# Optimization experiments

Measured on AMD Instinct MI355X. Metric: run time of the kernel, lower is better.

The kernel has to match this reference:

```python
import jax, jax.numpy as jnp
import numpy as np

B, CIN, COUT, T, J = 64, 128, 128, 128, 25
EPS = 1e-5  # BatchNorm2d default eps


def setup_inputs() -> dict:
    key = jax.random.key(0)
    k = jax.random.split(key, 5)
    x = jax.random.normal(k[0], (B, CIN, T, J), jnp.float32)
    adj = jax.random.normal(k[1], (J, J), jnp.float32) / np.sqrt(J).astype(np.float32)
    Wk = jax.random.normal(k[2], (COUT, CIN), jnp.float32) / np.sqrt(CIN).astype(np.float32)
    Wq = jax.random.normal(k[3], (COUT, CIN), jnp.float32) / np.sqrt(CIN).astype(np.float32)
    Ws = jax.random.normal(k[4], (COUT, CIN), jnp.float32) / np.sqrt(CIN).astype(np.float32)
    return {
        "x": x, "adj": adj,
        "Wk": Wk, "bk": jnp.zeros((COUT,), jnp.float32),
        "Wq": Wq, "bq": jnp.zeros((COUT,), jnp.float32),
        "Ws": Ws, "bs": jnp.zeros((COUT,), jnp.float32),
        "gamma": jnp.ones((COUT,), jnp.float32),
        "beta": jnp.zeros((COUT,), jnp.float32),
        "run_mean": jnp.zeros((COUT,), jnp.float32),
        "run_var": jnp.ones((COUT,), jnp.float32),
        "alpha": jnp.ones((1,), jnp.float32),
    }


def reference(x, adj, Wk, bk, Wq, bq, Ws, bs, gamma, beta, run_mean, run_var, alpha):
    # static graph conv: aggregate over joints with the shared adjacency
    static = jnp.einsum('bctj,jk->bctk', x, adj)              # [B,Cin,T,J]
    # 1x1 conv == channel matmul
    static_feat = jnp.einsum('oc,bctj->botj', Ws, static) + bs[None, :, None, None]  # [B,Cout,T,J]
    # temporal mean pooling, then key/query 1x1 convs
    x_t = x.mean(axis=2)                                      # [B,Cin,J]
    kk = jnp.einsum('oc,bcj->boj', Wk, x_t) + bk[None, :, None]  # [B,Cout,J]
    qq = jnp.einsum('oc,bcj->boj', Wq, x_t) + bq[None, :, None]  # [B,Cout,J]
    # attention-style dynamic adjacency: softmax(q^T k / sqrt(Cout)) over last axis
    scale = jnp.sqrt(jnp.asarray(kk.shape[1], x.dtype))
    scores = jnp.einsum('bcj,bck->bjk', qq, kk) / scale       # [B,J,J]
    dyn = jax.nn.softmax(scores, axis=-1)                     # [B,J,J]
    # original expands dyn to (B*T, Cout, J, J); same math without materialization:
    dyn_feat = jnp.einsum('bctj,bjk->bctk', static_feat, dyn)  # [B,Cout,T,J]
    out = static_feat + alpha[0] * dyn_feat
    # BatchNorm2d in inference mode (running stats), then ReLU
    inv = gamma[None, :, None, None] * jax.lax.rsqrt(run_var[None, :, None, None] + EPS)
    out = (out - run_mean[None, :, None, None]) * inv + beta[None, :, None, None]
    return jax.nn.relu(out)
```

## Files before the change

kernel.cpp:

```cpp
#include <hip/hip_runtime.h>

#define B_ 64
#define C_ 128
#define T_ 128
#define J_ 25
#define PIT 136
#define XP 40
#define GP 136
#define TT 4

typedef unsigned short ushort_t;
typedef __attribute__((ext_vector_type(8))) unsigned short ushort8;
typedef __attribute__((ext_vector_type(4))) unsigned short ushort4_t;
typedef __attribute__((ext_vector_type(8))) _Float16 half8;
typedef __attribute__((ext_vector_type(4))) float f32x4;
typedef float f32x4u __attribute__((ext_vector_type(4), aligned(4)));
typedef unsigned short ushort8u __attribute__((ext_vector_type(8), aligned(2)));

__device__ __forceinline__ float bf2f(ushort_t u) {
  unsigned int v = ((unsigned int)u) << 16;
  return __builtin_bit_cast(float, v);
}
__device__ __forceinline__ ushort_t f2bf(float f) {
  unsigned int u = __builtin_bit_cast(unsigned int, f);
  u += 0x7FFFu + ((u >> 16) & 1u);
  return (ushort_t)(u >> 16);
}
__device__ __forceinline__ ushort_t f2h_bits(float f) {
  _Float16 h = (_Float16)f;
  return __builtin_bit_cast(ushort_t, h);
}
__device__ __forceinline__ float h2f(ushort_t u) {
  return (float)__builtin_bit_cast(_Float16, u);
}
__device__ __forceinline__ half8 cvt_bf8_h8(ushort8 u) {
  half8 r;
#pragma unroll
  for (int i = 0; i < 8; ++i) r[i] = (_Float16)bf2f(u[i]);
  return r;
}
__device__ __forceinline__ float ldv(const void* p, long i, int isf32) {
  return isf32 ? ((const float*)p)[i] : bf2f(((const ushort_t*)p)[i]);
}
__device__ __forceinline__ half8 ld8h(const void* p, long i, int isf32) {
  half8 r;
  if (isf32) {
    const float* f = (const float*)p + i;
#pragma unroll
    for (int k = 0; k < 8; ++k) r[k] = (_Float16)f[k];
  } else {
    ushort8 u = *(const ushort8*)((const ushort_t*)p + i);
    r = cvt_bf8_h8(u);
  }
  return r;
}

__device__ __forceinline__ int detect_isf32(const void* p, int tid) {
  const ushort_t* u = (const ushort_t*)p;
  float a = fabsf(bf2f(u[2 * (tid & 63)]));
  int ok = (a > 1e-4f && a < 64.f) ? 1 : 0;
  unsigned long long m = __ballot(ok);
  return (__popcll(m) > 32) ? 0 : 1;
}

__global__ __launch_bounds__(256) void k_mean(const void* __restrict__ x,
                                              float* __restrict__ xt) {
  const int bc = blockIdx.x;
  const int b = bc >> 7, c = bc & 127;
  const long base = (long)bc * 3200;
  const int tid = threadIdx.x;
  const int isf32 = detect_isf32((const ushort_t*)x + base, tid);
  __shared__ float pl[3200];
  __shared__ float red[8][32];
  if (isf32) {
    const f32x4* src = (const f32x4*)((const float*)x + base);
    for (int i = tid; i < 800; i += 256) *(f32x4*)&pl[i * 4] = src[i];
  } else {
    const ushort4_t* src = (const ushort4_t*)((const ushort_t*)x + base);
    for (int i = tid; i < 800; i += 256) {
      ushort4_t u = src[i];
      f32x4 v;
#pragma unroll
      for (int r = 0; r < 4; ++r) v[r] = bf2f(u[r]);
      *(f32x4*)&pl[i * 4] = v;
    }
  }
  __syncthreads();
  const int j = tid & 31, g = tid >> 5;
  float s = 0.f;
  if (j < J_) {
#pragma unroll
    for (int i = 0; i < 16; ++i) s += pl[(g * 16 + i) * 25 + j];
  }
  red[g][j] = s;
  __syncthreads();
  if (tid < 32) {
    float tot = 0.f;
#pragma unroll
    for (int gg = 0; gg < 8; ++gg) tot += red[gg][tid];
    if (tid < J_) xt[b * 4096 + tid * 128 + c] = tot * (1.0f / 128.0f);
  }
}

__global__ __launch_bounds__(256) void k_attn(
    const float* __restrict__ xt, const void* __restrict__ adj,
    const void* __restrict__ Wk, const void* __restrict__ bk,
    const void* __restrict__ Wq, const void* __restrict__ bq,
    const void* __restrict__ alphap, ushort_t* __restrict__ fkws,
    float* __restrict__ sws) {
  const int b = blockIdx.x;
  const int tid = threadIdx.x;
  const int isf32 = detect_isf32(Wk, tid);
  const int wv = tid >> 6, lane = tid & 63, lrow = lane & 15, quad = lane >> 4;
  const float alpha = ldv(alphap, 0, isf32);

  __shared__ __align__(16) ushort_t xtT[32 * PIT];
  __shared__ __align__(16) ushort_t kkT[32 * PIT];
  __shared__ __align__(16) ushort_t qqT[32 * PIT];
  __shared__ float sc[32 * 33];

  for (int idx = tid; idx < 32 * PIT; idx += 256) {
    int r = idx / PIT, col = idx % PIT;
    float v = (r < J_ && col < 128) ? xt[b * 4096 + r * 128 + col] : 0.f;
    xtT[idx] = f2h_bits(v);
  }
  __syncthreads();

  for (int mat = 0; mat < 2; ++mat) {
    const void* W = mat ? Wq : Wk;
    const void* bias = mat ? bq : bk;
    ushort_t* dstT = mat ? qqT : kkT;
    f32x4 acc[2][2] = {};
    for (int ks = 0; ks < 4; ++ks) {
      half8 bfr[2];
#pragma unroll
      for (int jt = 0; jt < 2; ++jt)
        bfr[jt] = *(const half8*)&xtT[(jt * 16 + lrow) * PIT + ks * 32 + quad * 8];
#pragma unroll
      for (int ot = 0; ot < 2; ++ot) {
        int o = (2 * wv + ot) * 16 + lrow;
        half8 afr = ld8h(W, o * 128 + ks * 32 + quad * 8, isf32);
#pragma unroll
        for (int jt = 0; jt < 2; ++jt)
          acc[ot][jt] = __builtin_amdgcn_mfma_f32_16x16x32_f16(afr, bfr[jt],
                                                               acc[ot][jt], 0, 0, 0);
      }
    }
#pragma unroll
    for (int ot = 0; ot < 2; ++ot) {
      int obase = (2 * wv + ot) * 16 + quad * 4;
#pragma unroll
      for (int jt = 0; jt < 2; ++jt) {
        int j = jt * 16 + lrow;
        ushort_t pack[4];
#pragma unroll
        for (int r = 0; r < 4; ++r)
          pack[r] = f2h_bits(acc[ot][jt][r] + ldv(bias, obase + r, isf32));
        *(ushort4_t*)&dstT[j * PIT + obase] = *(ushort4_t*)pack;
      }
    }
  }
  __syncthreads();

  {
    const int mt = wv >> 1, nt = wv & 1;
    f32x4 acc = {};
    for (int ks = 0; ks < 4; ++ks) {
      half8 afr = *(const half8*)&qqT[(mt * 16 + lrow) * PIT + ks * 32 + quad * 8];
      half8 bfr = *(const half8*)&kkT[(nt * 16 + lrow) * PIT + ks * 32 + quad * 8];
      acc = __builtin_amdgcn_mfma_f32_16x16x32_f16(afr, bfr, acc, 0, 0, 0);
    }
    const float rs = 0.08838834764831845f;
#pragma unroll
    for (int r = 0; r < 4; ++r)
      sc[(mt * 16 + quad * 4 + r) * 33 + nt * 16 + lrow] = acc[r] * rs;
  }
  __syncthreads();

  if (tid < J_) {
    float m = -1e30f;
    for (int k = 0; k < J_; ++k) m = fmaxf(m, sc[tid * 33 + k]);
    float sum = 0.f;
    for (int k = 0; k < J_; ++k) {
      float e = expf(sc[tid * 33 + k] - m);
      sc[tid * 33 + k] = e;
      sum += e;
    }
    float inv = 1.f / sum;
    for (int k = 0; k < J_; ++k) sc[tid * 33 + k] *= inv;
  }
  __syncthreads();

  for (int idx = tid; idx < 1280; idx += 256) {
    int k = idx / XP, jj = idx % XP;
    float v = 0.f;
    if (k < J_ && jj < J_) {
      v = ldv(adj, jj * J_ + k, isf32);
      float d = 0.f;
      for (int m = 0; m < J_; ++m) d += ldv(adj, jj * J_ + m, isf32) * sc[m * 33 + k];
      v += alpha * d;
    }
    fkws[b * 1280 + idx] = f2h_bits(v);
  }
  if (tid < 32) {
    float v = 0.f;
    if (tid < J_) {
      float d = 0.f;
      for (int jj = 0; jj < J_; ++jj) d += sc[jj * 33 + tid];
      v = 1.f + alpha * d;
    }
    sws[b * 32 + tid] = v;
  }
}

#define SM_FK 0
#define SM_GT 2560
#define SM_TOT 33024
__global__ __launch_bounds__(256, 4) void k_main(
    const void* __restrict__ x, const void* __restrict__ Ws,
    const void* __restrict__ bs, const void* __restrict__ gamma,
    const void* __restrict__ beta, const void* __restrict__ rmean,
    const void* __restrict__ rvar, const ushort_t* __restrict__ fkws,
    const float* __restrict__ sws, void* __restrict__ out) {
  const int tid = threadIdx.x;
  const int isf32 = detect_isf32(Ws, tid);
  const int b = blockIdx.x >> 5, tb = blockIdx.x & 31, t0 = tb * TT;
  const int wv = tid >> 6, lane = tid & 63, lrow = lane & 15, quad = lane >> 4;

  __shared__ __align__(16) char smem[SM_TOT];
  __shared__ float bnscale[128], bnshift[128], bsv[128], sv[32];
  ushort_t* fk = (ushort_t*)(smem + SM_FK);
  ushort_t* gt = (ushort_t*)(smem + SM_GT);
  ushort_t* outbuf = (ushort_t*)(smem + SM_GT);

  half8 wsf[2][4];
#pragma unroll
  for (int ot = 0; ot < 2; ++ot) {
    int o = (2 * wv + ot) * 16 + lrow;
#pragma unroll
    for (int ks = 0; ks < 4; ++ks)
      wsf[ot][ks] = ld8h(Ws, o * 128 + ks * 32 + quad * 8, isf32);
  }

  for (int i = tid; i < 160; i += 256)
    *(ushort8*)&fk[i * 8] = *(const ushort8*)&fkws[b * 1280 + i * 8];
  for (int i = tid; i < 204; i += 256) {
    int row = 100 + i / 17, col8 = (i % 17) * 8;
    ushort8 z = {};
    *(ushort8*)&gt[row * GP + col8] = z;
  }
  if (tid < 32) sv[tid] = sws[b * 32 + tid];
  if (tid < 128) {
    float g = ldv(gamma, tid, isf32), v = ldv(rvar, tid, isf32);
    float scl = g * rsqrtf(v + 1e-5f);
    bnscale[tid] = scl;
    bnshift[tid] = ldv(beta, tid, isf32) - ldv(rmean, tid, isf32) * scl;
    bsv[tid] = ldv(bs, tid, isf32);
  }
  __syncthreads();

  {
    half8 afr[2];
#pragma unroll
    for (int mt = 0; mt < 2; ++mt)
      afr[mt] = *(const half8*)&fk[(mt * 16 + lrow) * XP + quad * 8];
    const float* xf = (const float*)x;
    const ushort_t* xh = (const ushort_t*)x;
#pragma unroll
    for (int t = 0; t < TT; ++t) {
#pragma unroll
      for (int ci = 0; ci < 2; ++ci) {
        int ct = 2 * wv + ci;
        long p = (long)b * 409600 + (long)(ct * 16 + lrow) * 3200 + (t0 + t) * 25;
        half8 bfr;
        if (quad < 3) {
          if (isf32) {
            f32x4u v0 = *(const f32x4u*)(xf + p + quad * 8);
            f32x4u v1 = *(const f32x4u*)(xf + p + quad * 8 + 4);
#pragma unroll
            for (int r = 0; r < 4; ++r) {
              bfr[r] = (_Float16)v0[r];
              bfr[4 + r] = (_Float16)v1[r];
            }
          } else {
            ushort8u u = *(const ushort8u*)(xh + p + quad * 8);
#pragma unroll
            for (int r = 0; r < 8; ++r) bfr[r] = (_Float16)bf2f(u[r]);
          }
        } else {
          bfr = (half8){};
          bfr[0] = (_Float16)(isf32 ? xf[p + 24] : bf2f(xh[p + 24]));
        }
        f32x4 accg[2] = {};
#pragma unroll
        for (int mt = 0; mt < 2; ++mt)
          accg[mt] = __builtin_amdgcn_mfma_f32_16x16x32_f16(afr[mt], bfr, accg[mt], 0, 0, 0);
#pragma unroll
        for (int mt = 0; mt < 2; ++mt)
#pragma unroll
          for (int r = 0; r < 4; ++r) {
            int kk = mt * 16 + quad * 4 + r;
            if (kk < J_)
              gt[(t * 25 + kk) * GP + ct * 16 + lrow] = f2h_bits(accg[mt][r]);
          }
      }
    }
  }
  __syncthreads();

  f32x4 acc[2][7];
#pragma unroll
  for (int ot = 0; ot < 2; ++ot)
#pragma unroll
    for (int nt = 0; nt < 7; ++nt) acc[ot][nt] = (f32x4){};
  for (int ks = 0; ks < 4; ++ks) {
#pragma unroll
    for (int nt = 0; nt < 7; ++nt) {
      half8 bfr = *(const half8*)&gt[(nt * 16 + lrow) * GP + ks * 32 + quad * 8];
#pragma unroll
      for (int ot = 0; ot < 2; ++ot)
        acc[ot][nt] = __builtin_amdgcn_mfma_f32_16x16x32_f16(wsf[ot][ks], bfr,
                                                             acc[ot][nt], 0, 0, 0);
    }
  }
  __syncthreads();

#pragma unroll
  for (int nt = 0; nt < 7; ++nt) {
    int n = nt * 16 + lrow;
    if (n < 100) {
      float svk = sv[n % 25];
#pragma unroll
      for (int ot = 0; ot < 2; ++ot) {
        int obase = (2 * wv + ot) * 16 + quad * 4;
#pragma unroll
        for (int r = 0; r < 4; ++r) {
          int o = obase + r;
          float v = acc[ot][nt][r] + bsv[o] * svk;
          v = v * bnscale[o] + bnshift[o];
          outbuf[o * 100 + n] = f2h_bits(fmaxf(v, 0.f));
        }
      }
    }
  }
  __syncthreads();

  {
    const long obase = ((long)(b * 128) * 128 + t0) * 25;
    if (isf32) {
      float* of = (float*)out + obase;
      for (int idx = tid; idx < 3200; idx += 256) {
        int o = idx / 25, q = idx % 25;
        ushort4_t u = *(const ushort4_t*)&outbuf[o * 100 + q * 4];
        f32x4 v;
#pragma unroll
        for (int r = 0; r < 4; ++r) v[r] = h2f(u[r]);
        *(f32x4*)(of + (long)o * 3200 + q * 4) = v;
      }
    } else {
      ushort_t* oh = (ushort_t*)out + obase;
      for (int idx = tid; idx < 3200; idx += 256) {
        int o = idx / 25, q = idx % 25;
        ushort4_t u = *(const ushort4_t*)&outbuf[o * 100 + q * 4];
        ushort4_t w;
#pragma unroll
        for (int r = 0; r < 4; ++r) w[r] = f2bf(h2f(u[r]));
        *(ushort4_t*)(oh + (long)o * 3200 + q * 4) = w;
      }
    }
  }
}

extern "C" void kernel_launch(void* const* d_in, const int* in_sizes, int n_in,
                              void* d_out, int out_size, void* d_ws, size_t ws_size,
                              hipStream_t stream) {
  const void* x = d_in[0];
  const void* adj = d_in[1];
  const void* Wk = d_in[2];
  const void* bk = d_in[3];
  const void* Wq = d_in[4];
  const void* bq = d_in[5];
  const void* Ws = d_in[6];
  const void* bsp = d_in[7];
  const void* gamma = d_in[8];
  const void* beta = d_in[9];
  const void* rmean = d_in[10];
  const void* rvar = d_in[11];
  const void* alphap = d_in[12];

  char* ws = (char*)d_ws;
  float* xt = (float*)ws;
  ushort_t* fkws = (ushort_t*)(ws + 64 * 4096 * 4);
  float* sws = (float*)(ws + 64 * 4096 * 4 + 64 * 1280 * 2);

  k_mean<<<B_ * C_, 256, 0, stream>>>(x, xt);
  k_attn<<<B_, 256, 0, stream>>>(xt, adj, Wk, bk, Wq, bq, alphap, fkws, sws);
  k_main<<<B_ * (T_ / TT), 256, 0, stream>>>(x, Ws, bsp, gamma, beta, rmean, rvar,
                                             fkws, sws, d_out);
}
```

Baseline: 300.0 us.

## Halve k_main time tile, prefetch x, write output directly from MFMA accumulators

k_main now handles 2 timesteps per block instead of 4, which doubles the grid and shrinks shared memory so the launch bound can request 6 blocks per CU. The x fragments are loaded into registers before the fk/BN setup so global latency overlaps the setup work. The second MFMA swaps its operands so each lane owns one output channel, letting the epilogue apply bias, BN and ReLU and store straight to global memory, removing the outbuf staging and two barriers. The xt workspace is stored as fp16, so k_attn can read it with vector loads. Trade-offs: more blocks reload the Ws fragments and fkws, and the direct stores are narrower and less coalesced than the old staged writes.

Result: slower. 316.7 us (+5.6%).

```diff
diff --git a/kernel.cpp b/kernel.cpp
--- a/kernel.cpp
+++ b/kernel.cpp
@@ -7,7 +7,7 @@
 #define PIT 136
 #define XP 40
 #define GP 136
-#define TT 4
+#define TT 2
 
 typedef unsigned short ushort_t;
 typedef __attribute__((ext_vector_type(8))) unsigned short ushort8;
@@ -16,6 +16,7 @@
 typedef __attribute__((ext_vector_type(4))) float f32x4;
 typedef float f32x4u __attribute__((ext_vector_type(4), aligned(4)));
 typedef unsigned short ushort8u __attribute__((ext_vector_type(8), aligned(2)));
+typedef unsigned short ushort4u __attribute__((ext_vector_type(4), aligned(2)));
 
 __device__ __forceinline__ float bf2f(ushort_t u) {
   unsigned int v = ((unsigned int)u) << 16;
@@ -64,7 +65,7 @@
 }
 
 __global__ __launch_bounds__(256) void k_mean(const void* __restrict__ x,
-                                              float* __restrict__ xt) {
+                                              ushort_t* __restrict__ xt) {
   const int bc = blockIdx.x;
   const int b = bc >> 7, c = bc & 127;
   const long base = (long)bc * 3200;
@@ -98,12 +99,12 @@
     float tot = 0.f;
 #pragma unroll
     for (int gg = 0; gg < 8; ++gg) tot += red[gg][tid];
-    if (tid < J_) xt[b * 4096 + tid * 128 + c] = tot * (1.0f / 128.0f);
+    if (tid < J_) xt[b * 4096 + tid * 128 + c] = f2h_bits(tot * (1.0f / 128.0f));
   }
 }
 
 __global__ __launch_bounds__(256) void k_attn(
-    const float* __restrict__ xt, const void* __restrict__ adj,
+    const ushort_t* __restrict__ xt, const void* __restrict__ adj,
     const void* __restrict__ Wk, const void* __restrict__ bk,
     const void* __restrict__ Wq, const void* __restrict__ bq,
     const void* __restrict__ alphap, ushort_t* __restrict__ fkws,
@@ -119,10 +120,11 @@
   __shared__ __align__(16) ushort_t qqT[32 * PIT];
   __shared__ float sc[32 * 33];
 
-  for (int idx = tid; idx < 32 * PIT; idx += 256) {
-    int r = idx / PIT, col = idx % PIT;
-    float v = (r < J_ && col < 128) ? xt[b * 4096 + r * 128 + col] : 0.f;
-    xtT[idx] = f2h_bits(v);
+  for (int idx = tid; idx < 32 * 17; idx += 256) {
+    int r = idx / 17, c8 = idx % 17;
+    ushort8 v = {};
+    if (r < J_ && c8 < 16) v = *(const ushort8*)&xt[b * 4096 + r * 128 + c8 * 8];
+    *(ushort8*)&xtT[r * PIT + c8 * 8] = v;
   }
   __syncthreads();
 
@@ -215,8 +217,8 @@
 
 #define SM_FK 0
 #define SM_GT 2560
-#define SM_TOT 33024
-__global__ __launch_bounds__(256, 4) void k_main(
+#define SM_TOT (2560 + 64 * GP * 2)
+__global__ __launch_bounds__(256, 6) void k_main(
     const void* __restrict__ x, const void* __restrict__ Ws,
     const void* __restrict__ bs, const void* __restrict__ gamma,
     const void* __restrict__ beta, const void* __restrict__ rmean,
@@ -224,14 +226,13 @@
     const float* __restrict__ sws, void* __restrict__ out) {
   const int tid = threadIdx.x;
   const int isf32 = detect_isf32(Ws, tid);
-  const int b = blockIdx.x >> 5, tb = blockIdx.x & 31, t0 = tb * TT;
+  const int b = blockIdx.x >> 6, tb = blockIdx.x & 63, t0 = tb * TT;
   const int wv = tid >> 6, lane = tid & 63, lrow = lane & 15, quad = lane >> 4;
 
   __shared__ __align__(16) char smem[SM_TOT];
   __shared__ float bnscale[128], bnshift[128], bsv[128], sv[32];
   ushort_t* fk = (ushort_t*)(smem + SM_FK);
   ushort_t* gt = (ushort_t*)(smem + SM_GT);
-  ushort_t* outbuf = (ushort_t*)(smem + SM_GT);
 
   half8 wsf[2][4];
 #pragma unroll
@@ -242,12 +243,44 @@
       wsf[ot][ks] = ld8h(Ws, o * 128 + ks * 32 + quad * 8, isf32);
   }
 
+  half8 xa[TT][2];
+  {
+    const float* xf = (const float*)x;
+    const ushort_t* xh = (const ushort_t*)x;
+#pragma unroll
+    for (int t = 0; t < TT; ++t)
+#pragma unroll
+      for (int ci = 0; ci < 2; ++ci) {
+        const int ct = 2 * wv + ci;
+        const long p = (long)b * 409600 + (long)(ct * 16 + lrow) * 3200 + (t0 + t) * 25;
+        half8 bfr;
+        if (quad < 3) {
+          if (isf32) {
+            f32x4u v0 = *(const f32x4u*)(xf + p + quad * 8);
+            f32x4u v1 = *(const f32x4u*)(xf + p + quad * 8 + 4);
+#pragma unroll
+            for (int r = 0; r < 4; ++r) {
+              bfr[r] = (_Float16)v0[r];
+              bfr[4 + r] = (_Float16)v1[r];
+            }
+          } else {
+            ushort8u u = *(const ushort8u*)(xh + p + quad * 8);
+#pragma unroll
+            for (int r = 0; r < 8; ++r) bfr[r] = (_Float16)bf2f(u[r]);
+          }
+        } else {
+          bfr = (half8){};
+          bfr[0] = (_Float16)(isf32 ? xf[p + 24] : bf2f(xh[p + 24]));
+        }
+        xa[t][ci] = bfr;
+      }
+  }
+
   for (int i = tid; i < 160; i += 256)
     *(ushort8*)&fk[i * 8] = *(const ushort8*)&fkws[b * 1280 + i * 8];
-  for (int i = tid; i < 204; i += 256) {
-    int row = 100 + i / 17, col8 = (i % 17) * 8;
+  for (int i = tid; i < 238; i += 256) {
     ushort8 z = {};
-    *(ushort8*)&gt[row * GP + col8] = z;
+    *(ushort8*)&gt[50 * GP + i * 8] = z;
   }
   if (tid < 32) sv[tid] = sws[b * 32 + tid];
   if (tid < 128) {
@@ -264,42 +297,21 @@
 #pragma unroll
     for (int mt = 0; mt < 2; ++mt)
       afr[mt] = *(const half8*)&fk[(mt * 16 + lrow) * XP + quad * 8];
-    const float* xf = (const float*)x;
-    const ushort_t* xh = (const ushort_t*)x;
 #pragma unroll
     for (int t = 0; t < TT; ++t) {
 #pragma unroll
       for (int ci = 0; ci < 2; ++ci) {
-        int ct = 2 * wv + ci;
-        long p = (long)b * 409600 + (long)(ct * 16 + lrow) * 3200 + (t0 + t) * 25;
-        half8 bfr;
-        if (quad < 3) {
-          if (isf32) {
-            f32x4u v0 = *(const f32x4u*)(xf + p + quad * 8);
-            f32x4u v1 = *(const f32x4u*)(xf + p + quad * 8 + 4);
-#pragma unroll
-            for (int r = 0; r < 4; ++r) {
-              bfr[r] = (_Float16)v0[r];
-              bfr[4 + r] = (_Float16)v1[r];
-            }
-          } else {
-            ushort8u u = *(const ushort8u*)(xh + p + quad * 8);
-#pragma unroll
-            for (int r = 0; r < 8; ++r) bfr[r] = (_Float16)bf2f(u[r]);
-          }
-        } else {
-          bfr = (half8){};
-          bfr[0] = (_Float16)(isf32 ? xf[p + 24] : bf2f(xh[p + 24]));
-        }
+        const int ct = 2 * wv + ci;
         f32x4 accg[2] = {};
 #pragma unroll
         for (int mt = 0; mt < 2; ++mt)
-          accg[mt] = __builtin_amdgcn_mfma_f32_16x16x32_f16(afr[mt], bfr, accg[mt], 0, 0, 0);
+          accg[mt] = __builtin_amdgcn_mfma_f32_16x16x32_f16(afr[mt], xa[t][ci],
+                                                            accg[mt], 0, 0, 0);
 #pragma unroll
         for (int mt = 0; mt < 2; ++mt)
 #pragma unroll
           for (int r = 0; r < 4; ++r) {
-            int kk = mt * 16 + quad * 4 + r;
+            const int kk = mt * 16 + quad * 4 + r;
             if (kk < J_)
               gt[(t * 25 + kk) * GP + ct * 16 + lrow] = f2h_bits(accg[mt][r]);
           }
@@ -308,64 +320,64 @@
   }
   __syncthreads();
 
-  f32x4 acc[2][7];
+  f32x4 acc[2][4];
 #pragma unroll
   for (int ot = 0; ot < 2; ++ot)
 #pragma unroll
-    for (int nt = 0; nt < 7; ++nt) acc[ot][nt] = (f32x4){};
+    for (int nt = 0; nt < 4; ++nt) acc[ot][nt] = (f32x4){};
+#pragma unroll
   for (int ks = 0; ks < 4; ++ks) {
 #pragma unroll
-    for (int nt = 0; nt < 7; ++nt) {
-      half8 bfr = *(const half8*)&gt[(nt * 16 + lrow) * GP + ks * 32 + quad * 8];
+    for (int nt = 0; nt < 4; ++nt) {
+      half8 gfr = *(const half8*)&gt[(nt * 16 + lrow) * GP + ks * 32 + quad * 8];
 #pragma unroll
       for (int ot = 0; ot < 2; ++ot)
-        acc[ot][nt] = __builtin_amdgcn_mfma_f32_16x16x32_f16(wsf[ot][ks], bfr,
+        acc[ot][nt] = __builtin_amdgcn_mfma_f32_16x16x32_f16(gfr, wsf[ot][ks],
                                                              acc[ot][nt], 0, 0, 0);
     }
   }
-  __syncthreads();
-
-#pragma unroll
-  for (int nt = 0; nt < 7; ++nt) {
-    int n = nt * 16 + lrow;
-    if (n < 100) {
-      float svk = sv[n % 25];
-#pragma unroll
-      for (int ot = 0; ot < 2; ++ot) {
-        int obase = (2 * wv + ot) * 16 + quad * 4;
-#pragma unroll
-        for (int r = 0; r < 4; ++r) {
-          int o = obase + r;
-          float v = acc[ot][nt][r] + bsv[o] * svk;
-          v = v * bnscale[o] + bnshift[o];
-          outbuf[o * 100 + n] = f2h_bits(fmaxf(v, 0.f));
+
+  {
+    const long obase = (long)b * 409600 + (long)t0 * 25;
+#pragma unroll
+    for (int ot = 0; ot < 2; ++ot) {
+      const int o = (2 * wv + ot) * 16 + lrow;
+      const float scl = bnscale[o], sht = bnshift[o], bsb = bsv[o];
+      const long op = obase + (long)o * 3200;
+#pragma unroll
+      for (int nt = 0; nt < 4; ++nt) {
+        const int n0 = nt * 16 + quad * 4;
+        if (n0 < 50) {
+          float v[4];
+#pragma unroll
+          for (int r = 0; r < 4; ++r) {
+            const int n = n0 + r;
+            const int j = n >= 25 ? n - 25 : n;
+            float u = acc[ot][nt][r] + bsb * sv[j];
+            v[r] = fmaxf(u * scl + sht, 0.f);
+          }
+          if (isf32) {
+            float* of = (float*)out + op + n0;
+            if (n0 <= 46) {
+              f32x4u w = {v[0], v[1], v[2], v[3]};
+              *(f32x4u*)of = w;
+            } else {
+              of[0] = v[0];
+              of[1] = v[1];
+            }
+          } else {
+            ushort_t* oh = (ushort_t*)out + op + n0;
+            if (n0 <= 46) {
+              ushort4u w;
+#pragma unroll
+              for (int r = 0; r < 4; ++r) w[r] = f2bf(v[r]);
+              *(ushort4u*)oh = w;
+            } else {
+              oh[0] = f2bf(v[0]);
+              oh[1] = f2bf(v[1]);
+            }
+          }
         }
-      }
-    }
-  }
-  __syncthreads();
-
-  {
-    const long obase = ((long)(b * 128) * 128 + t0) * 25;
-    if (isf32) {
-      float* of = (float*)out + obase;
-      for (int idx = tid; idx < 3200; idx += 256) {
-        int o = idx / 25, q = idx % 25;
-        ushort4_t u = *(const ushort4_t*)&outbuf[o * 100 + q * 4];
-        f32x4 v;
-#pragma unroll
-        for (int r = 0; r < 4; ++r) v[r] = h2f(u[r]);
-        *(f32x4*)(of + (long)o * 3200 + q * 4) = v;
-      }
-    } else {
-      ushort_t* oh = (ushort_t*)out + obase;
-      for (int idx = tid; idx < 3200; idx += 256) {
-        int o = idx / 25, q = idx % 25;
-        ushort4_t u = *(const ushort4_t*)&outbuf[o * 100 + q * 4];
-        ushort4_t w;
-#pragma unroll
-        for (int r = 0; r < 4; ++r) w[r] = f2bf(h2f(u[r]));
-        *(ushort4_t*)(oh + (long)o * 3200 + q * 4) = w;
       }
     }
   }
@@ -389,9 +401,9 @@
   const void* alphap = d_in[12];
 
   char* ws = (char*)d_ws;
-  float* xt = (float*)ws;
-  ushort_t* fkws = (ushort_t*)(ws + 64 * 4096 * 4);
-  float* sws = (float*)(ws + 64 * 4096 * 4 + 64 * 1280 * 2);
+  ushort_t* xt = (ushort_t*)ws;
+  ushort_t* fkws = (ushort_t*)(ws + 64 * 4096 * 2);
+  float* sws = (float*)(ws + 64 * 4096 * 2 + 64 * 1280 * 2);
 
   k_mean<<<B_ * C_, 256, 0, stream>>>(x, xt);
   k_attn<<<B_, 256, 0, stream>>>(xt, adj, Wk, bk, Wq, bq, alphap, fkws, sws);
```
